# Kernel tuning notes

Measured on AMD Instinct MI355X. Metric: run time of the kernel, lower is better.

## Reference

```python
import jax, jax.numpy as jnp
import numpy as np

NVOC, NIN, NHID = 50257, 1024, 1024
H2 = 2 * NHID  # AttLSTMBlock internal hidden size (cat of h_prev and context)


def setup_inputs() -> dict:
    key = jax.random.key(0)
    ks = jax.random.split(key, 12)
    T, B = 1024, 64
    return {
        "inputs": jax.random.randint(ks[0], (1, B), 0, NVOC),
        "memory_pool": jax.random.normal(ks[1], (T, B, NHID), jnp.float32),
        "h_prev": jax.random.normal(ks[2], (1, B, NHID), jnp.float32),
        "c_prev": jax.random.normal(ks[3], (1, B, H2), jnp.float32),
        "enc_w": jax.random.uniform(ks[4], (NVOC, NIN), jnp.float32, -0.1, 0.1),
        "attWa": jax.random.uniform(ks[5], (NHID, NHID), jnp.float32, -0.1, 0.1),
        "attUa": jax.random.uniform(ks[6], (NHID, NHID), jnp.float32, -0.1, 0.1),
        "attV": jax.random.normal(ks[7], (NHID,), jnp.float32) * 0.1,
        "W_ih": jax.random.normal(ks[8], (NIN, 4 * H2), jnp.float32) * 0.02,
        "W_hh": jax.random.normal(ks[9], (H2, 4 * H2), jnp.float32) * 0.02,
        "b_lstm": jnp.zeros((4 * H2,), jnp.float32),
        "dec_w": jax.random.uniform(ks[10], (NVOC, NHID), jnp.float32, -0.1, 0.1),
        "dec_b": jnp.zeros((NVOC,), jnp.float32),
    }


def reference(inputs, memory_pool, h_prev, c_prev, enc_w, attWa, attUa, attV,
              W_ih, W_hh, b_lstm, dec_w, dec_b):
    # Embedding lookup (dropout = identity in eval mode): [1,B,NIN]
    emb = enc_w[inputs]
    # Bahdanau additive attention: score [T,B], softmax over T (dim=0)
    score = jnp.tanh(h_prev @ attWa + memory_pool @ attUa) @ attV  # [T,B] (h_prev broadcasts over T)
    attWeight = jax.nn.softmax(score, axis=0)
    contextVec = jnp.sum(attWeight[:, :, None] * memory_pool, axis=0)  # [B,NHID]
    att_h = jnp.concatenate([h_prev, contextVec[None]], axis=2)  # [1,B,2*NHID]
    # LSTM cell step with hidden size H2
    gates = emb @ W_ih + att_h @ W_hh + b_lstm  # [1,B,4*H2]
    i, f, g, o = jnp.split(gates, 4, axis=-1)
    ct = jax.nn.sigmoid(f) * c_prev + jax.nn.sigmoid(i) * jnp.tanh(g)
    ht_full = jax.nn.sigmoid(o) * jnp.tanh(ct)
    ht = ht_full[:, :, :NHID]  # slice back to nhid
    # Linear decode
    B = ht.shape[1]
    decoded = (ht.reshape(B, NHID) @ dec_w.T + dec_b).reshape(1, B, NVOC)
    return decoded.squeeze(0), ht, ct
```

## Files before the change

kernel.cpp:

```cpp
#include <hip/hip_runtime.h>

#define T_LEN 1024
#define BATCH 64
#define NHID  1024
#define H2    2048
#define NVOC  50257
#define G4    8192
#define KCAT  3072
#define LS    56

typedef __attribute__((ext_vector_type(4))) float  f4;
typedef __attribute__((ext_vector_type(4))) float  f32x4;
typedef __attribute__((ext_vector_type(8))) __bf16 bf8;
typedef __attribute__((ext_vector_type(4))) __bf16 bf4;

__device__ inline float fast_tanh(float x) {
    float e = __expf(2.0f * x);
    return 1.0f - 2.0f / (e + 1.0f);
}
__device__ inline float fast_sig(float x) {
    return 1.0f / (1.0f + __expf(-x));
}

__global__ __launch_bounds__(256) void transpose_ua(const float* __restrict__ ua,
                                                    __bf16* __restrict__ uaT) {
    __shared__ float tile[64][65];
    const int tid = threadIdx.x;
    const int kb = (blockIdx.x & 15) * 64, nb = (blockIdx.x >> 4) * 64;
#pragma unroll
    for (int i = 0; i < 16; ++i) {
        int idx = tid + 256 * i;
        int kr = idx >> 6, nc = idx & 63;
        tile[kr][nc] = ua[(size_t)(kb + kr) * NHID + nb + nc];
    }
    __syncthreads();
#pragma unroll
    for (int i = 0; i < 16; ++i) {
        int idx = tid + 256 * i;
        int nr = idx >> 6, kc = idx & 63;
        uaT[(size_t)(nb + nr) * NHID + kb + kc] = (__bf16)tile[kc][nr];
    }
}

__global__ void prep_emb_h(const int* __restrict__ inp, const float* __restrict__ enc,
                           const float* __restrict__ h, __bf16* __restrict__ Ag) {
    const int b = blockIdx.x, tid = threadIdx.x;
    const int tok = inp[b];
#pragma unroll
    for (int i = 0; i < 4; ++i) {
        int n = tid + 256 * i;
        Ag[(size_t)b * KCAT + n]        = (__bf16)enc[(size_t)tok * NHID + n];
        Ag[(size_t)b * KCAT + NHID + n] = (__bf16)h[(size_t)b * NHID + n];
    }
}

__global__ __launch_bounds__(256) void small_gemm(
    const __bf16* __restrict__ A, int lda, int K, int k1,
    const float* __restrict__ B1, const float* __restrict__ B2, int ldb,
    float* __restrict__ out, int ldo, int mode) {
    __shared__ __bf16 As[64 * LS];
    __shared__ __bf16 Bs[64 * LS];
    const int tid = threadIdx.x;
    const int lane = tid & 63, wave = tid >> 6;
    const int quad = lane >> 4, l15 = lane & 15;
    const int n0 = blockIdx.x * 64;
    const int ar = tid >> 2, ac = (tid & 3) * 8;

    f32x4 acc[4] = {};

    for (int k0 = 0; k0 < K; k0 += 32) {
        __syncthreads();
        *(bf8*)&As[ar * LS + ac] = *(const bf8*)(A + (size_t)ar * lda + k0 + ac);
#pragma unroll
        for (int j = 0; j < 2; ++j) {
            int idx = tid + 256 * j;
            int kr = idx >> 4, nc = (idx & 15) * 4;
            int kg = k0 + kr;
            const float* src = (kg < k1) ? (B1 + (size_t)kg * ldb)
                                         : (B2 + (size_t)(kg - k1) * ldb);
            f4 v = *(const f4*)(src + n0 + nc);
#pragma unroll
            for (int i = 0; i < 4; ++i) Bs[(nc + i) * LS + kr] = (__bf16)v[i];
        }
        __syncthreads();
        bf8 bfr = *(const bf8*)&Bs[(wave * 16 + l15) * LS + quad * 8];
#pragma unroll
        for (int mi = 0; mi < 4; ++mi) {
            bf8 af = *(const bf8*)&As[(mi * 16 + l15) * LS + quad * 8];
            acc[mi] = __builtin_amdgcn_mfma_f32_16x16x32_bf16(af, bfr, acc[mi], 0, 0, 0);
        }
    }
    const int n = n0 + wave * 16 + l15;
    if (mode == 0) {
#pragma unroll
        for (int mi = 0; mi < 4; ++mi)
#pragma unroll
            for (int r = 0; r < 4; ++r)
                out[(size_t)(mi * 16 + quad * 4 + r) * ldo + n] = acc[mi][r];
    } else {
#pragma unroll
        for (int mi = 0; mi < 4; ++mi)
            *(f4*)&out[(size_t)n * 64 + mi * 16 + quad * 4] = acc[mi];
    }
}

__global__ __launch_bounds__(256) void score_gemm(
    const float* __restrict__ mem, const __bf16* __restrict__ uaT,
    const float* __restrict__ hWaT, const float* __restrict__ attV,
    float* __restrict__ scoreT) {
    __shared__ __bf16 As[128 * LS];
    __shared__ __bf16 Bs[128 * LS];
    const int tid = threadIdx.x;
    const int lane = tid & 63, wave = tid >> 6;
    const int wM = wave >> 1, wN = wave & 1;
    const int quad = lane >> 4, l15 = lane & 15;
    const int mb = blockIdx.x >> 3, nb = blockIdx.x & 7;
    const int n0 = nb * 128;

    const int arow = tid >> 1, ahalf = (tid & 1) * 16;
    const float*  aptr = mem + (size_t)(mb * 128 + arow) * NHID + ahalf;
    const __bf16* bptr = uaT + (size_t)(n0 + arow) * NHID + ahalf;

    f4  ga[4];
    bf8 gb[2];
#pragma unroll
    for (int j = 0; j < 4; ++j) ga[j] = *(const f4*)(aptr + 4 * j);
#pragma unroll
    for (int j = 0; j < 2; ++j) gb[j] = *(const bf8*)(bptr + 8 * j);

    f32x4 acc[4][4] = {};

    for (int k0 = 0; k0 < NHID; k0 += 32) {
        __syncthreads();
#pragma unroll
        for (int j = 0; j < 4; ++j) {
            bf4 w;
            w[0] = (__bf16)ga[j][0]; w[1] = (__bf16)ga[j][1];
            w[2] = (__bf16)ga[j][2]; w[3] = (__bf16)ga[j][3];
            *(bf4*)&As[arow * LS + ahalf + 4 * j] = w;
        }
#pragma unroll
        for (int j = 0; j < 2; ++j) *(bf8*)&Bs[arow * LS + ahalf + 8 * j] = gb[j];
        __syncthreads();
        if (k0 + 32 < NHID) {
#pragma unroll
            for (int j = 0; j < 4; ++j) ga[j] = *(const f4*)(aptr + k0 + 32 + 4 * j);
#pragma unroll
            for (int j = 0; j < 2; ++j) gb[j] = *(const bf8*)(bptr + k0 + 32 + 8 * j);
        }
        bf8 af[4], bfr[4];
#pragma unroll
        for (int i = 0; i < 4; ++i)
            af[i] = *(const bf8*)&As[(wM * 64 + i * 16 + l15) * LS + quad * 8];
#pragma unroll
        for (int i = 0; i < 4; ++i)
            bfr[i] = *(const bf8*)&Bs[(wN * 64 + i * 16 + l15) * LS + quad * 8];
#pragma unroll
        for (int mi = 0; mi < 4; ++mi)
#pragma unroll
            for (int ni = 0; ni < 4; ++ni)
                acc[mi][ni] = __builtin_amdgcn_mfma_f32_16x16x32_bf16(
                    af[mi], bfr[ni], acc[mi][ni], 0, 0, 0);
    }

    const int tglob = mb * 2 + wM;
#pragma unroll
    for (int mi = 0; mi < 4; ++mi) {
        float rs[4] = {0.f, 0.f, 0.f, 0.f};
#pragma unroll
        for (int ni = 0; ni < 4; ++ni) {
            int n = n0 + wN * 64 + ni * 16 + l15;
            f4 hw = *(const f4*)&hWaT[(size_t)n * 64 + mi * 16 + quad * 4];
            float av = attV[n];
#pragma unroll
            for (int r = 0; r < 4; ++r)
                rs[r] += fast_tanh(acc[mi][ni][r] + hw[r]) * av;
        }
#pragma unroll
        for (int r = 0; r < 4; ++r) {
            float v = rs[r];
            v += __shfl_xor(v, 1); v += __shfl_xor(v, 2);
            v += __shfl_xor(v, 4); v += __shfl_xor(v, 8);
            if (l15 == 0) {
                int b = mi * 16 + quad * 4 + r;
                atomicAdd(&scoreT[b * T_LEN + tglob], v);
            }
        }
    }
}

__global__ void softmax_k(const float* __restrict__ scoreT, float* __restrict__ wts) {
    const int b = blockIdx.x, tid = threadIdx.x;
    const int lane = tid & 63, wave = tid >> 6;
    __shared__ float red[4];
    __shared__ float red2[4];
    float s[4];
    float mx = -1e30f;
#pragma unroll
    for (int i = 0; i < 4; ++i) {
        s[i] = scoreT[b * T_LEN + tid + 256 * i];
        mx = fmaxf(mx, s[i]);
    }
#pragma unroll
    for (int o = 1; o < 64; o <<= 1) mx = fmaxf(mx, __shfl_xor(mx, o));
    if (lane == 0) red[wave] = mx;
    __syncthreads();
    mx = fmaxf(fmaxf(red[0], red[1]), fmaxf(red[2], red[3]));
    float e[4], sum = 0.f;
#pragma unroll
    for (int i = 0; i < 4; ++i) { e[i] = __expf(s[i] - mx); sum += e[i]; }
#pragma unroll
    for (int o = 1; o < 64; o <<= 1) sum += __shfl_xor(sum, o);
    if (lane == 0) red2[wave] = sum;
    __syncthreads();
    sum = red2[0] + red2[1] + red2[2] + red2[3];
    float inv = 1.0f / sum;
#pragma unroll
    for (int i = 0; i < 4; ++i) wts[b * T_LEN + tid + 256 * i] = e[i] * inv;
}

__global__ void context_k(const float* __restrict__ wts, const float* __restrict__ mem,
                          float* __restrict__ ctx) {
    const int b = blockIdx.x >> 3, tc = blockIdx.x & 7;
    const int n4 = threadIdx.x * 4;
    f4 acc = {0.f, 0.f, 0.f, 0.f};
    const int t0 = tc * 128;
    for (int t = t0; t < t0 + 128; ++t) {
        float w = wts[b * T_LEN + t];
        f4 m = *(const f4*)(mem + ((size_t)t * BATCH + b) * NHID + n4);
        acc += w * m;
    }
#pragma unroll
    for (int i = 0; i < 4; ++i) atomicAdd(&ctx[(size_t)b * NHID + n4 + i], acc[i]);
}

__global__ void ctx_cvt(const float* __restrict__ ctx, __bf16* __restrict__ Ag) {
    const int b = blockIdx.x, tid = threadIdx.x;
#pragma unroll
    for (int i = 0; i < 4; ++i) {
        int n = tid + 256 * i;
        Ag[(size_t)b * KCAT + H2 + n] = (__bf16)ctx[(size_t)b * NHID + n];
    }
}

__global__ void lstm_k(const float* __restrict__ gates, const float* __restrict__ bl,
                       const float* __restrict__ cprev, float* __restrict__ out_ct,
                       float* __restrict__ out_ht, __bf16* __restrict__ htb) {
    const int idx = blockIdx.x * 256 + threadIdx.x;
    const int b = idx >> 11, k = idx & 2047;
    float gi = gates[(size_t)b * G4 + k]          + bl[k];
    float gf = gates[(size_t)b * G4 + H2 + k]     + bl[H2 + k];
    float gg = gates[(size_t)b * G4 + 2 * H2 + k] + bl[2 * H2 + k];
    float go = gates[(size_t)b * G4 + 3 * H2 + k] + bl[3 * H2 + k];
    float ct = fast_sig(gf) * cprev[idx] + fast_sig(gi) * fast_tanh(gg);
    float ht = fast_sig(go) * fast_tanh(ct);
    out_ct[idx] = ct;
    if (k < NHID) {
        out_ht[(size_t)b * NHID + k] = ht;
        htb[(size_t)b * NHID + k]    = (__bf16)ht;
    }
}

__global__ __launch_bounds__(256) void dec_gemm(
    const __bf16* __restrict__ htb, const float* __restrict__ dw,
    const float* __restrict__ db, float* __restrict__ outd) {
    __shared__ __bf16 As[64 * LS];
    __shared__ __bf16 Bs[128 * LS];
    const int tid = threadIdx.x;
    const int lane = tid & 63, wave = tid >> 6;
    const int quad = lane >> 4, l15 = lane & 15;
    const int n0 = blockIdx.x * 128;
    const int ar = tid >> 2, ac = (tid & 3) * 8;
    const int br = tid >> 1, bc = (tid & 1) * 16;
    const int vrow = n0 + br;

    f32x4 acc[4][2] = {};

    for (int k0 = 0; k0 < NHID; k0 += 32) {
        __syncthreads();
        *(bf8*)&As[ar * LS + ac] = *(const bf8*)(htb + (size_t)ar * NHID + k0 + ac);
#pragma unroll
        for (int j = 0; j < 4; ++j) {
            f4 v = {0.f, 0.f, 0.f, 0.f};
            if (vrow < NVOC) v = *(const f4*)(dw + (size_t)vrow * NHID + k0 + bc + 4 * j);
            bf4 w;
            w[0] = (__bf16)v[0]; w[1] = (__bf16)v[1];
            w[2] = (__bf16)v[2]; w[3] = (__bf16)v[3];
            *(bf4*)&Bs[br * LS + bc + 4 * j] = w;
        }
        __syncthreads();
#pragma unroll
        for (int ni = 0; ni < 2; ++ni) {
            bf8 bfr = *(const bf8*)&Bs[(wave * 32 + ni * 16 + l15) * LS + quad * 8];
#pragma unroll
            for (int mi = 0; mi < 4; ++mi) {
                bf8 af = *(const bf8*)&As[(mi * 16 + l15) * LS + quad * 8];
                acc[mi][ni] = __builtin_amdgcn_mfma_f32_16x16x32_bf16(af, bfr, acc[mi][ni], 0, 0, 0);
            }
        }
    }
#pragma unroll
    for (int ni = 0; ni < 2; ++ni) {
        int n = n0 + wave * 32 + ni * 16 + l15;
        if (n < NVOC) {
            float bb = db[n];
#pragma unroll
            for (int mi = 0; mi < 4; ++mi)
#pragma unroll
                for (int r = 0; r < 4; ++r)
                    outd[(size_t)(mi * 16 + quad * 4 + r) * NVOC + n] = acc[mi][ni][r] + bb;
        }
    }
}

extern "C" void kernel_launch(void* const* d_in, const int* in_sizes, int n_in,
                              void* d_out, int out_size, void* d_ws, size_t ws_size,
                              hipStream_t stream) {
    (void)in_sizes; (void)n_in; (void)out_size; (void)ws_size;
    const int*   inp   = (const int*)d_in[0];
    const float* mem   = (const float*)d_in[1];
    const float* hprev = (const float*)d_in[2];
    const float* cprev = (const float*)d_in[3];
    const float* encw  = (const float*)d_in[4];
    const float* attWa = (const float*)d_in[5];
    const float* attUa = (const float*)d_in[6];
    const float* attV  = (const float*)d_in[7];
    const float* Wih   = (const float*)d_in[8];
    const float* Whh   = (const float*)d_in[9];
    const float* blstm = (const float*)d_in[10];
    const float* decw  = (const float*)d_in[11];
    const float* decb  = (const float*)d_in[12];

    char* ws = (char*)d_ws;
    float*  scoreT = (float*)(ws);
    float*  wts    = (float*)(ws + 262144);
    float*  hWaT   = (float*)(ws + 524288);
    float*  ctx    = (float*)(ws + 786432);
    float*  gates  = (float*)(ws + 1048576);
    __bf16* Ag     = (__bf16*)(ws + 3145728);
    __bf16* htb    = (__bf16*)(ws + 3538944);
    __bf16* uaT    = (__bf16*)(ws + 3670016);

    float* outdec = (float*)d_out;
    float* outht  = outdec + (size_t)BATCH * NVOC;
    float* outct  = outht + BATCH * NHID;

    hipMemsetAsync(scoreT, 0, 262144, stream);
    hipMemsetAsync(ctx, 0, 262144, stream);
    hipLaunchKernelGGL(transpose_ua, dim3(256), dim3(256), 0, stream, attUa, uaT);
    hipLaunchKernelGGL(prep_emb_h, dim3(64), dim3(256), 0, stream, inp, encw, hprev, Ag);
    hipLaunchKernelGGL(small_gemm, dim3(16), dim3(256), 0, stream,
                       Ag + NHID, KCAT, NHID, NHID, attWa, attWa, NHID, hWaT, 64, 1);
    hipLaunchKernelGGL(score_gemm, dim3(4096), dim3(256), 0, stream,
                       mem, uaT, hWaT, attV, scoreT);
    hipLaunchKernelGGL(softmax_k, dim3(64), dim3(256), 0, stream, scoreT, wts);
    hipLaunchKernelGGL(context_k, dim3(512), dim3(256), 0, stream, wts, mem, ctx);
    hipLaunchKernelGGL(ctx_cvt, dim3(64), dim3(256), 0, stream, ctx, Ag);
    hipLaunchKernelGGL(small_gemm, dim3(128), dim3(256), 0, stream,
                       Ag, KCAT, KCAT, NHID, Wih, Whh, G4, gates, G4, 0);
    hipLaunchKernelGGL(lstm_k, dim3(512), dim3(256), 0, stream,
                       gates, blstm, cprev, outct, outht, htb);
    hipLaunchKernelGGL(dec_gemm, dim3((NVOC + 127) / 128), dim3(256), 0, stream,
                       htb, decw, decb, outdec);
}
```

Measured before the change: 1.219 ms.

## Pre-convert memory pool to bf16 and stream score GEMM tiles via direct global-to-LDS loads

Adds a conversion kernel that writes the 256MB fp32 memory pool to a bf16 workspace copy. A new score GEMM then loads A and B tiles straight into LDS with global_load_lds, dropping the register staging and in-loop conversion, and remaps block indices so groups of M-tiles share N-tiles. The old fp32 path stays as a fallback when the workspace is too small. The price is an extra full pass over the memory pool (read 256MB, write 128MB) and a loop that no longer prefetches the next tile while computing the current one.

Result: faster. 1.176 ms (-3.5%).

```diff
diff --git a/kernel.cpp b/kernel.cpp
--- a/kernel.cpp
+++ b/kernel.cpp
@@ -14,12 +14,26 @@
 typedef __attribute__((ext_vector_type(8))) __bf16 bf8;
 typedef __attribute__((ext_vector_type(4))) __bf16 bf4;
 
+#define GPTR(p) ((const __attribute__((address_space(1))) void*)(p))
+#define LPTR(p) ((__attribute__((address_space(3))) void*)(p))
+
 __device__ inline float fast_tanh(float x) {
     float e = __expf(2.0f * x);
     return 1.0f - 2.0f / (e + 1.0f);
 }
 __device__ inline float fast_sig(float x) {
     return 1.0f / (1.0f + __expf(-x));
+}
+
+__global__ __launch_bounds__(256) void cvt_mem(const float* __restrict__ mem,
+                                               __bf16* __restrict__ memb) {
+    const size_t i = ((size_t)blockIdx.x * 256 + threadIdx.x) * 8;
+    f4 a = *(const f4*)(mem + i);
+    f4 b = *(const f4*)(mem + i + 4);
+    bf8 w;
+    w[0] = (__bf16)a[0]; w[1] = (__bf16)a[1]; w[2] = (__bf16)a[2]; w[3] = (__bf16)a[3];
+    w[4] = (__bf16)b[0]; w[5] = (__bf16)b[1]; w[6] = (__bf16)b[2]; w[7] = (__bf16)b[3];
+    *(bf8*)(memb + i) = w;
 }
 
 __global__ __launch_bounds__(256) void transpose_ua(const float* __restrict__ ua,
@@ -105,6 +119,79 @@
 }
 
 __global__ __launch_bounds__(256) void score_gemm(
+    const __bf16* __restrict__ memb, const __bf16* __restrict__ uaT,
+    const float* __restrict__ hWaT, const float* __restrict__ attV,
+    float* __restrict__ scoreT) {
+    __shared__ __bf16 As[128 * 32];
+    __shared__ __bf16 Bs[128 * 32];
+    const int tid = threadIdx.x;
+    const int lane = tid & 63, wave = tid >> 6;
+    const int wM = wave >> 1, wN = wave & 1;
+    const int quad = lane >> 4, l15 = lane & 15;
+    const int bidx = blockIdx.x;
+    const int mb = (bidx >> 6) * 8 + (bidx & 7);
+    const int nb = (bidx >> 3) & 7;
+    const int n0 = nb * 128, m0 = mb * 128;
+
+    const int srow = lane >> 2, scol = (lane & 3) * 8;
+
+    f32x4 acc[4][4] = {};
+
+    for (int k0 = 0; k0 < NHID; k0 += 32) {
+        __syncthreads();
+#pragma unroll
+        for (int j = 0; j < 2; ++j) {
+            const int c = wave * 2 + j;
+            __builtin_amdgcn_global_load_lds(
+                GPTR(memb + (size_t)(m0 + c * 16 + srow) * NHID + k0 + scol),
+                LPTR(As + c * 512), 16, 0, 0);
+            __builtin_amdgcn_global_load_lds(
+                GPTR(uaT + (size_t)(n0 + c * 16 + srow) * NHID + k0 + scol),
+                LPTR(Bs + c * 512), 16, 0, 0);
+        }
+        __syncthreads();
+        bf8 af[4], bfr[4];
+#pragma unroll
+        for (int i = 0; i < 4; ++i)
+            af[i] = *(const bf8*)&As[(wM * 64 + i * 16 + l15) * 32 + quad * 8];
+#pragma unroll
+        for (int i = 0; i < 4; ++i)
+            bfr[i] = *(const bf8*)&Bs[(wN * 64 + i * 16 + l15) * 32 + quad * 8];
+#pragma unroll
+        for (int mi = 0; mi < 4; ++mi)
+#pragma unroll
+            for (int ni = 0; ni < 4; ++ni)
+                acc[mi][ni] = __builtin_amdgcn_mfma_f32_16x16x32_bf16(
+                    af[mi], bfr[ni], acc[mi][ni], 0, 0, 0);
+    }
+
+    const int tglob = mb * 2 + wM;
+#pragma unroll
+    for (int mi = 0; mi < 4; ++mi) {
+        float rs[4] = {0.f, 0.f, 0.f, 0.f};
+#pragma unroll
+        for (int ni = 0; ni < 4; ++ni) {
+            int n = n0 + wN * 64 + ni * 16 + l15;
+            f4 hw = *(const f4*)&hWaT[(size_t)n * 64 + mi * 16 + quad * 4];
+            float av = attV[n];
+#pragma unroll
+            for (int r = 0; r < 4; ++r)
+                rs[r] += fast_tanh(acc[mi][ni][r] + hw[r]) * av;
+        }
+#pragma unroll
+        for (int r = 0; r < 4; ++r) {
+            float v = rs[r];
+            v += __shfl_xor(v, 1); v += __shfl_xor(v, 2);
+            v += __shfl_xor(v, 4); v += __shfl_xor(v, 8);
+            if (l15 == 0) {
+                int b = mi * 16 + quad * 4 + r;
+                atomicAdd(&scoreT[b * T_LEN + tglob], v);
+            }
+        }
+    }
+}
+
+__global__ __launch_bounds__(256) void score_gemm_f32(
     const float* __restrict__ mem, const __bf16* __restrict__ uaT,
     const float* __restrict__ hWaT, const float* __restrict__ attV,
     float* __restrict__ scoreT) {
@@ -116,20 +203,16 @@
     const int quad = lane >> 4, l15 = lane & 15;
     const int mb = blockIdx.x >> 3, nb = blockIdx.x & 7;
     const int n0 = nb * 128;
-
     const int arow = tid >> 1, ahalf = (tid & 1) * 16;
     const float*  aptr = mem + (size_t)(mb * 128 + arow) * NHID + ahalf;
     const __bf16* bptr = uaT + (size_t)(n0 + arow) * NHID + ahalf;
-
     f4  ga[4];
     bf8 gb[2];
 #pragma unroll
     for (int j = 0; j < 4; ++j) ga[j] = *(const f4*)(aptr + 4 * j);
 #pragma unroll
     for (int j = 0; j < 2; ++j) gb[j] = *(const bf8*)(bptr + 8 * j);
-
     f32x4 acc[4][4] = {};
-
     for (int k0 = 0; k0 < NHID; k0 += 32) {
         __syncthreads();
 #pragma unroll
@@ -162,7 +245,6 @@
                 acc[mi][ni] = __builtin_amdgcn_mfma_f32_16x16x32_bf16(
                     af[mi], bfr[ni], acc[mi][ni], 0, 0, 0);
     }
-
     const int tglob = mb * 2 + wM;
 #pragma unroll
     for (int mi = 0; mi < 4; ++mi) {
@@ -316,7 +398,7 @@
 extern "C" void kernel_launch(void* const* d_in, const int* in_sizes, int n_in,
                               void* d_out, int out_size, void* d_ws, size_t ws_size,
                               hipStream_t stream) {
-    (void)in_sizes; (void)n_in; (void)out_size; (void)ws_size;
+    (void)in_sizes; (void)n_in; (void)out_size;
     const int*   inp   = (const int*)d_in[0];
     const float* mem   = (const float*)d_in[1];
     const float* hprev = (const float*)d_in[2];
@@ -340,6 +422,8 @@
     __bf16* Ag     = (__bf16*)(ws + 3145728);
     __bf16* htb    = (__bf16*)(ws + 3538944);
     __bf16* uaT    = (__bf16*)(ws + 3670016);
+    __bf16* memb   = (__bf16*)(ws + 5767168);
+    const size_t ws_need = 5767168 + (size_t)T_LEN * BATCH * NHID * 2;
 
     float* outdec = (float*)d_out;
     float* outht  = outdec + (size_t)BATCH * NVOC;
@@ -351,8 +435,14 @@
     hipLaunchKernelGGL(prep_emb_h, dim3(64), dim3(256), 0, stream, inp, encw, hprev, Ag);
     hipLaunchKernelGGL(small_gemm, dim3(16), dim3(256), 0, stream,
                        Ag + NHID, KCAT, NHID, NHID, attWa, attWa, NHID, hWaT, 64, 1);
-    hipLaunchKernelGGL(score_gemm, dim3(4096), dim3(256), 0, stream,
-                       mem, uaT, hWaT, attV, scoreT);
+    if (ws_size >= ws_need) {
+        hipLaunchKernelGGL(cvt_mem, dim3(32768), dim3(256), 0, stream, mem, memb);
+        hipLaunchKernelGGL(score_gemm, dim3(4096), dim3(256), 0, stream,
+                           memb, uaT, hWaT, attV, scoreT);
+    } else {
+        hipLaunchKernelGGL(score_gemm_f32, dim3(4096), dim3(256), 0, stream,
+                           mem, uaT, hWaT, attV, scoreT);
+    }
     hipLaunchKernelGGL(softmax_k, dim3(64), dim3(256), 0, stream, scoreT, wts);
     hipLaunchKernelGGL(context_k, dim3(512), dim3(256), 0, stream, wts, mem, ctx);
     hipLaunchKernelGGL(ctx_cvt, dim3(64), dim3(256), 0, stream, ctx, Ag);
```
